# Performance work log

Measured on AMD Instinct MI355X. Metric: run time of the kernel, lower is better.

## Reference

```python
import jax, jax.numpy as jnp
import numpy as np

L_SEQ = 4096   # sequence length L
E = 1024       # embedding_size
NL = 8         # num_layers
H = 4 * E      # channel-mix hidden
V = 4          # LocalHilDim
LOGP_FACTOR = 0.5


def setup_inputs() -> dict:
    key = jax.random.key(0)
    ks = jax.random.split(key, 20)
    n = lambda k, shp, s=0.02: jax.random.normal(k, shp, jnp.float32) * s
    u = lambda k, shp: jax.random.uniform(k, shp, dtype=jnp.float32)
    return {
        "s": jax.random.randint(ks[0], (L_SEQ,), 0, V),
        "embed": n(ks[1], (V, E), 1.0),
        # TimeMixing params, stacked over layers
        "tm_first": jnp.log(jnp.float32(0.3)) + n(ks[2], (NL, E), 0.5),
        "tm_decay": -5.0 + 8.0 * u(ks[3], (NL, E)),
        "tm_mk": u(ks[4], (NL, E)),
        "tm_mv": u(ks[5], (NL, E)),
        "tm_mr": u(ks[6], (NL, E)),
        "tm_Wk": n(ks[7], (NL, E, E)),
        "tm_Wv": n(ks[8], (NL, E, E)),
        "tm_Wr": n(ks[9], (NL, E, E)),
        "tm_Wo": n(ks[10], (NL, E, E)),
        # ChannelMixing params
        "cm_mk": u(ks[11], (NL, E)),
        "cm_mr": u(ks[12], (NL, E)),
        "cm_Wk": n(ks[13], (NL, E, H)),
        "cm_Wr": n(ks[14], (NL, E, E)),
        "cm_Wv": n(ks[15], (NL, H, E)),
        # Neck / Head
        "neck_W": n(ks[16], (E, E)),
        "neck_b": jnp.zeros((E,), jnp.float32),
        "head_W": n(ks[17], (E, V)),
    }


def _wkv(k, v, time_first, time_decay):
    """Max-stabilized RWKV WKV recurrence over time. k,v: [L,E]."""
    z = jnp.zeros_like(k[0])
    init = (z, z, jnp.full_like(k[0], -jnp.inf))  # aa, bb, pp

    def step(carry, kv):
        aa, bb, pp = carry
        kk, vv = kv
        ww = time_first + kk
        p = jnp.maximum(pp, ww)
        e1 = jnp.exp(pp - p)
        e2 = jnp.exp(ww - p)
        out = (e1 * aa + e2 * vv) / (e1 * bb + e2)
        ww = pp - jnp.exp(time_decay)
        p = jnp.maximum(ww, kk)
        e1 = jnp.exp(ww - p)
        e2 = jnp.exp(kk - p)
        return (e1 * aa + e2 * vv, e1 * bb + e2, p), out

    _, out = jax.lax.scan(step, init, (k, v))
    return out


def _shift(x):
    # prepend zero-state row, drop last (token-shift with zero initial state)
    return jnp.concatenate([jnp.zeros_like(x[:1]), x[:-1]], axis=0)


def _block(x, p):
    # --- TimeMixing ---
    sx = _shift(x)
    kx = x * p["tm_mk"] + sx * (1 - p["tm_mk"])
    vx = x * p["tm_mv"] + sx * (1 - p["tm_mv"])
    rx = x * p["tm_mr"] + sx * (1 - p["tm_mr"])
    r = jax.nn.sigmoid(rx @ p["tm_Wr"])
    k = kx @ p["tm_Wk"]
    v = vx @ p["tm_Wv"]
    wkv = _wkv(k, v, p["tm_first"], p["tm_decay"])
    x = x + (r * wkv) @ p["tm_Wo"]
    # --- ChannelMixing ---
    sx = _shift(x)
    xk = x * p["cm_mk"] + sx * (1 - p["cm_mk"])
    xr = x * p["cm_mr"] + sx * (1 - p["cm_mr"])
    r = jax.nn.sigmoid(xr @ p["cm_Wr"])
    kk = jnp.square(jax.nn.relu(xk @ p["cm_Wk"]))  # [L, 4E]
    x = x + r * (kk @ p["cm_Wv"])
    return x


def reference(s, embed, tm_first, tm_decay, tm_mk, tm_mv, tm_mr,
              tm_Wk, tm_Wv, tm_Wr, tm_Wo, cm_mk, cm_mr, cm_Wk, cm_Wr, cm_Wv,
              neck_W, neck_b, head_W):
    tok = jnp.pad(s[:-1], (1, 0))
    x = embed[tok]                          # [L, E]
    layer_params = {
        "tm_first": tm_first, "tm_decay": tm_decay,
        "tm_mk": tm_mk, "tm_mv": tm_mv, "tm_mr": tm_mr,
        "tm_Wk": tm_Wk, "tm_Wv": tm_Wv, "tm_Wr": tm_Wr, "tm_Wo": tm_Wo,
        "cm_mk": cm_mk, "cm_mr": cm_mr,
        "cm_Wk": cm_Wk, "cm_Wr": cm_Wr, "cm_Wv": cm_Wv,
    }

    def body(x, p):
        return _block(x, p), None

    x, _ = jax.lax.scan(body, x, layer_params)  # scan over NL layers
    x = jax.nn.gelu(x @ neck_W + neck_b)
    logits = x @ head_W                         # [L, V]
    logp = jax.nn.log_softmax(logits) * LOGP_FACTOR
    # log-amplitude of configuration s (Q is None -> no mask, no penalty)
    return jnp.take_along_axis(logp, s[:, None], axis=-1).sum(axis=-2).squeeze(-1)
```

## Files before the change

### kernel.cpp

```cpp
#include <hip/hip_runtime.h>
#include <stdint.h>

#define L_SEQ 4096
#define EDIM  1024
#define HDIM  4096
#define NLAY  8
#define WKV_C 128
#define WKV_T 32
#define SCAN_LANES 16
#define SCAN_CPT   (WKV_C / SCAN_LANES)

typedef unsigned short u16;
typedef __attribute__((ext_vector_type(8))) short short8;
typedef __attribute__((ext_vector_type(4))) float f32x4;
typedef __attribute__((ext_vector_type(4))) unsigned short us4;
typedef __attribute__((ext_vector_type(8))) unsigned short us8;

static __device__ __forceinline__ u16 f2b(float f) {
  union { float f; uint32_t u; } a; a.f = f;
  uint32_t u = a.u;
  return (u16)((u + 0x7FFFu + ((u >> 16) & 1u)) >> 16);
}
static __device__ __forceinline__ float b2f(u16 b) {
  union { uint32_t u; float f; } a; a.u = ((uint32_t)b) << 16;
  return a.f;
}
static __device__ __forceinline__ float sigm(float v) {
  return 1.f / (1.f + __expf(-v));
}
static __device__ __forceinline__ float4 ld_bf4(const u16* __restrict__ p, size_t i) {
  us4 v = *reinterpret_cast<const us4*>(&p[i]);
  return make_float4(b2f(v.x), b2f(v.y), b2f(v.z), b2f(v.w));
}

static __device__ __forceinline__ void gld_lds16(const void* g, void* l) {
  __builtin_amdgcn_global_load_lds(
      (const __attribute__((address_space(1))) void*)g,
      (__attribute__((address_space(3))) void*)l, 16, 0, 0);
}


__global__ void k_f0(const int* __restrict__ s, const float* __restrict__ embed,
                     const float* __restrict__ mk, const float* __restrict__ mv,
                     const float* __restrict__ mr, u16* __restrict__ xA,
                     u16* __restrict__ kx, u16* __restrict__ vx, u16* __restrict__ rx) {
  int i = (blockIdx.x * blockDim.x + threadIdx.x) * 4;
  int t = i >> 10, e = i & 1023;
  int tok = (t == 0) ? 0 : s[t - 1];
  float4 xc = *reinterpret_cast<const float4*>(&embed[tok * EDIM + e]);
  float4 xs = make_float4(0.f, 0.f, 0.f, 0.f);
  if (t > 0) {
    int tokp = (t == 1) ? 0 : s[t - 2];
    xs = *reinterpret_cast<const float4*>(&embed[tokp * EDIM + e]);
  }
  us4 ox; ox.x = f2b(xc.x); ox.y = f2b(xc.y); ox.z = f2b(xc.z); ox.w = f2b(xc.w);
  *reinterpret_cast<us4*>(&xA[i]) = ox;
  float4 m; us4 o;
  m = *reinterpret_cast<const float4*>(&mk[e]);
  o.x = f2b(xc.x * m.x + xs.x * (1.f - m.x)); o.y = f2b(xc.y * m.y + xs.y * (1.f - m.y));
  o.z = f2b(xc.z * m.z + xs.z * (1.f - m.z)); o.w = f2b(xc.w * m.w + xs.w * (1.f - m.w));
  *reinterpret_cast<us4*>(&kx[i]) = o;
  m = *reinterpret_cast<const float4*>(&mv[e]);
  o.x = f2b(xc.x * m.x + xs.x * (1.f - m.x)); o.y = f2b(xc.y * m.y + xs.y * (1.f - m.y));
  o.z = f2b(xc.z * m.z + xs.z * (1.f - m.z)); o.w = f2b(xc.w * m.w + xs.w * (1.f - m.w));
  *reinterpret_cast<us4*>(&vx[i]) = o;
  m = *reinterpret_cast<const float4*>(&mr[e]);
  o.x = f2b(xc.x * m.x + xs.x * (1.f - m.x)); o.y = f2b(xc.y * m.y + xs.y * (1.f - m.y));
  o.z = f2b(xc.z * m.z + xs.z * (1.f - m.z)); o.w = f2b(xc.w * m.w + xs.w * (1.f - m.w));
  *reinterpret_cast<us4*>(&rx[i]) = o;
}

static __device__ __forceinline__ float4 cm_finish(const u16* __restrict__ xB,
                                                   const u16* __restrict__ PR,
                                                   const u16* __restrict__ PB, int i) {
  const size_t LE = (size_t)L_SEQ * EDIM;
  float4 xm = ld_bf4(xB, i);
  float4 r0 = ld_bf4(PR, i), r1 = ld_bf4(PR, i + LE);
  float4 v0 = ld_bf4(PB, i), v1 = ld_bf4(PB, i + LE);
  float4 v2 = ld_bf4(PB, i + 2 * LE), v3 = ld_bf4(PB, i + 3 * LE);
  xm.x += sigm(r0.x + r1.x) * (v0.x + v1.x + v2.x + v3.x);
  xm.y += sigm(r0.y + r1.y) * (v0.y + v1.y + v2.y + v3.y);
  xm.z += sigm(r0.z + r1.z) * (v0.z + v1.z + v2.z + v3.z);
  xm.w += sigm(r0.w + r1.w) * (v0.w + v1.w + v2.w + v3.w);
  return xm;
}

__global__ void k_f1(const u16* __restrict__ xB, const u16* __restrict__ PR,
                     const u16* __restrict__ PB,
                     const float* __restrict__ mk, const float* __restrict__ mv,
                     const float* __restrict__ mr, u16* __restrict__ xA,
                     u16* __restrict__ kx, u16* __restrict__ vx, u16* __restrict__ rx) {
  int i = (blockIdx.x * blockDim.x + threadIdx.x) * 4;
  int e = i & 1023;
  float4 xc = cm_finish(xB, PR, PB, i);
  float4 xs = make_float4(0.f, 0.f, 0.f, 0.f);
  if (i >= EDIM) xs = cm_finish(xB, PR, PB, i - EDIM);
  us4 ox; ox.x = f2b(xc.x); ox.y = f2b(xc.y); ox.z = f2b(xc.z); ox.w = f2b(xc.w);
  *reinterpret_cast<us4*>(&xA[i]) = ox;
  float4 m; us4 o;
  m = *reinterpret_cast<const float4*>(&mk[e]);
  o.x = f2b(xc.x * m.x + xs.x * (1.f - m.x)); o.y = f2b(xc.y * m.y + xs.y * (1.f - m.y));
  o.z = f2b(xc.z * m.z + xs.z * (1.f - m.z)); o.w = f2b(xc.w * m.w + xs.w * (1.f - m.w));
  *reinterpret_cast<us4*>(&kx[i]) = o;
  m = *reinterpret_cast<const float4*>(&mv[e]);
  o.x = f2b(xc.x * m.x + xs.x * (1.f - m.x)); o.y = f2b(xc.y * m.y + xs.y * (1.f - m.y));
  o.z = f2b(xc.z * m.z + xs.z * (1.f - m.z)); o.w = f2b(xc.w * m.w + xs.w * (1.f - m.w));
  *reinterpret_cast<us4*>(&vx[i]) = o;
  m = *reinterpret_cast<const float4*>(&mr[e]);
  o.x = f2b(xc.x * m.x + xs.x * (1.f - m.x)); o.y = f2b(xc.y * m.y + xs.y * (1.f - m.y));
  o.z = f2b(xc.z * m.z + xs.z * (1.f - m.z)); o.w = f2b(xc.w * m.w + xs.w * (1.f - m.w));
  *reinterpret_cast<us4*>(&rx[i]) = o;
}

static __device__ __forceinline__ float4 tm_finish(const u16* __restrict__ xA,
                                                   const u16* __restrict__ PA, int i) {
  const size_t LE = (size_t)L_SEQ * EDIM;
  float4 xm = ld_bf4(xA, i);
  float4 a = ld_bf4(PA, i), b = ld_bf4(PA, i + LE);
  xm.x += a.x + b.x; xm.y += a.y + b.y; xm.z += a.z + b.z; xm.w += a.w + b.w;
  return xm;
}

__global__ void k_f2(const u16* __restrict__ xA, const u16* __restrict__ PA,
                     const float* __restrict__ mk, const float* __restrict__ mr,
                     u16* __restrict__ xB, u16* __restrict__ kx, u16* __restrict__ rx) {
  int i = (blockIdx.x * blockDim.x + threadIdx.x) * 4;
  int e = i & 1023;
  float4 xc = tm_finish(xA, PA, i);
  float4 xs = make_float4(0.f, 0.f, 0.f, 0.f);
  if (i >= EDIM) xs = tm_finish(xA, PA, i - EDIM);
  us4 ox; ox.x = f2b(xc.x); ox.y = f2b(xc.y); ox.z = f2b(xc.z); ox.w = f2b(xc.w);
  *reinterpret_cast<us4*>(&xB[i]) = ox;
  float4 m; us4 o;
  m = *reinterpret_cast<const float4*>(&mk[e]);
  o.x = f2b(xc.x * m.x + xs.x * (1.f - m.x)); o.y = f2b(xc.y * m.y + xs.y * (1.f - m.y));
  o.z = f2b(xc.z * m.z + xs.z * (1.f - m.z)); o.w = f2b(xc.w * m.w + xs.w * (1.f - m.w));
  *reinterpret_cast<us4*>(&kx[i]) = o;
  m = *reinterpret_cast<const float4*>(&mr[e]);
  o.x = f2b(xc.x * m.x + xs.x * (1.f - m.x)); o.y = f2b(xc.y * m.y + xs.y * (1.f - m.y));
  o.z = f2b(xc.z * m.z + xs.z * (1.f - m.z)); o.w = f2b(xc.w * m.w + xs.w * (1.f - m.w));
  *reinterpret_cast<us4*>(&rx[i]) = o;
}

__global__ void k_f3(const u16* __restrict__ xB, const u16* __restrict__ PR,
                     const u16* __restrict__ PB, u16* __restrict__ hb) {
  int i = (blockIdx.x * blockDim.x + threadIdx.x) * 4;
  float4 xc = cm_finish(xB, PR, PB, i);
  us4 o;
  o.x = f2b(xc.x); o.y = f2b(xc.y); o.z = f2b(xc.z); o.w = f2b(xc.w);
  *reinterpret_cast<us4*>(&hb[i]) = o;
}

static __device__ __forceinline__ float gelu1(float v) {
  float c = 0.7978845608028654f * (v + 0.044715f * v * v * v);
  return 0.5f * v * (1.f + tanhf(c));
}

static __device__ __forceinline__
void tconv2(const float* __restrict__ s, u16* __restrict__ d, int K, int N,
            int n0, int k0) {
  __shared__ float tile[64][65];
  int tid = threadIdx.x;
  int tx = tid & 15, ty = tid >> 4;
#pragma unroll
  for (int i = 0; i < 4; ++i) {
    int kr = ty + i * 16;
    float4 v = *reinterpret_cast<const float4*>(&s[(size_t)(k0 + kr) * N + n0 + tx * 4]);
    tile[kr][tx * 4 + 0] = v.x; tile[kr][tx * 4 + 1] = v.y;
    tile[kr][tx * 4 + 2] = v.z; tile[kr][tx * 4 + 3] = v.w;
  }
  __syncthreads();
  int tx8 = tid & 7, ny = tid >> 3;
#pragma unroll
  for (int h = 0; h < 2; ++h) {
    int n = ny + h * 32;
    us8 o;
#pragma unroll
    for (int c = 0; c < 8; ++c) o[c] = f2b(tile[tx8 * 8 + c][n]);
    *reinterpret_cast<us8*>(&d[(size_t)(n0 + n) * K + k0 + tx8 * 8]) = o;
  }
}

__global__ __launch_bounds__(256)
void k_tconv(const float* __restrict__ src, u16* __restrict__ dst, int K, int N) {
  tconv2(src + (size_t)blockIdx.z * K * N, dst + (size_t)blockIdx.z * K * N,
         K, N, blockIdx.x * 64, blockIdx.y * 64);
}

#define TC_EE  (41 * 256)
#define TC_EH  8192
__global__ __launch_bounds__(256)
void k_tconv_all(const float* __restrict__ Wk, const float* __restrict__ Wv,
                 const float* __restrict__ Wr, const float* __restrict__ Wo,
                 const float* __restrict__ cWr, const float* __restrict__ nW,
                 const float* __restrict__ cWk, const float* __restrict__ cWv,
                 u16* __restrict__ oWk, u16* __restrict__ oWv, u16* __restrict__ oWr,
                 u16* __restrict__ oWo, u16* __restrict__ ocWr, u16* __restrict__ onW,
                 u16* __restrict__ ocWk, u16* __restrict__ ocWv) {
  const size_t EE = (size_t)EDIM * EDIM, EH = (size_t)EDIM * HDIM;
  int bid = blockIdx.x;
  if (bid < TC_EE) {
    int z = bid >> 8, rem = bid & 255;
    const float* src; u16* dst;
    if (z < 8)       { src = Wk  + (size_t)z * EE;        dst = oWk  + (size_t)z * EE; }
    else if (z < 16) { src = Wv  + (size_t)(z - 8) * EE;  dst = oWv  + (size_t)(z - 8) * EE; }
    else if (z < 24) { src = Wr  + (size_t)(z - 16) * EE; dst = oWr  + (size_t)(z - 16) * EE; }
    else if (z < 32) { src = Wo  + (size_t)(z - 24) * EE; dst = oWo  + (size_t)(z - 24) * EE; }
    else if (z < 40) { src = cWr + (size_t)(z - 32) * EE; dst = ocWr + (size_t)(z - 32) * EE; }
    else             { src = nW;                          dst = onW; }
    tconv2(src, dst, EDIM, EDIM, (rem & 15) * 64, (rem >> 4) * 64);
  } else if (bid < TC_EE + TC_EH) {
    int b = bid - TC_EE;
    int z = b >> 10, rem = b & 1023;
    tconv2(cWk + (size_t)z * EH, ocWk + (size_t)z * EH, EDIM, HDIM,
           (rem & 63) * 64, (rem >> 6) * 64);
  } else {
    int b = bid - TC_EE - TC_EH;
    int z = b >> 10, rem = b & 1023;
    tconv2(cWv + (size_t)z * EH, ocWv + (size_t)z * EH, HDIM, EDIM,
           (rem & 15) * 64, (rem >> 4) * 64);
  }
}

template <int EPI>
__device__ __forceinline__
void g256_body(const u16* __restrict__ A, const u16* __restrict__ Bt,
               void* __restrict__ Cv, int N, int ldk, int klen,
               int bm, int bn) {
  extern __shared__ __align__(16) u16 lds[];
  const int tid = threadIdx.x, lane = tid & 63, w = tid >> 6;
  const int wr = w >> 2, wc = w & 3;
  const int l16 = lane & 15, lhi = lane >> 4;
  const int NT = klen >> 5;

  f32x4 acc[8][4];
#pragma unroll
  for (int i = 0; i < 8; ++i)
#pragma unroll
    for (int j = 0; j < 4; ++j)
#pragma unroll
      for (int r = 0; r < 4; ++r) acc[i][j][r] = 0.f;

  const int sd = tid * 16;
  const int sr = sd >> 6;
  const int sc = ((sd >> 4) & 3) ^ ((sr >> 1) & 3);
  const int sdst = w * 512;

  const int spn = lhi ^ ((l16 >> 1) & 3);
  const int aBase = wr * 4096 + l16 * 32 + spn * 8;
  const int bBase = 8192 + (wc >> 1) * 4096 + ((wc & 1) * 64 + l16) * 32 + spn * 8;

  auto stage_ht = [&](int kt, int ht) {
    const u16* src = (ht < 2) ? A : Bt;
    int rowbase = ((ht < 2) ? bm : bn) + (ht & 1) * 128;
    gld_lds16(src + (size_t)(rowbase + sr) * ldk + kt * 32 + sc * 8,
              &lds[(kt & 3) * 16384 + ht * 4096 + sdst]);
  };

#pragma unroll
  for (int t = 0; t < 3; ++t)
#pragma unroll
    for (int h = 0; h < 4; ++h) stage_ht(t, h);
  asm volatile("s_waitcnt vmcnt(8)" ::: "memory");
  __builtin_amdgcn_s_barrier();

  short8 a[4], b[4];
  for (int kt = 0; kt < NT; ++kt) {
    const int pb = (kt & 3) * 16384;
    __builtin_amdgcn_sched_barrier(0);
#pragma unroll
    for (int mi = 0; mi < 4; ++mi)
      a[mi] = *reinterpret_cast<const short8*>(&lds[pb + aBase + mi * 512]);
#pragma unroll
    for (int ni = 0; ni < 4; ++ni)
      b[ni] = *reinterpret_cast<const short8*>(&lds[pb + bBase + ni * 512]);
    if (kt + 3 < NT) { stage_ht(kt + 3, 0); stage_ht(kt + 3, 1); }
    __builtin_amdgcn_s_barrier();
    asm volatile("s_waitcnt lgkmcnt(0)" ::: "memory");
    __builtin_amdgcn_sched_barrier(0);
    __builtin_amdgcn_s_setprio(1);
#pragma unroll
    for (int mi = 0; mi < 4; ++mi)
#pragma unroll
      for (int ni = 0; ni < 4; ++ni)
        acc[mi][ni] = __builtin_amdgcn_mfma_f32_16x16x32_bf16(a[mi], b[ni], acc[mi][ni], 0, 0, 0);
    __builtin_amdgcn_s_setprio(0);
    __builtin_amdgcn_s_barrier();
    __builtin_amdgcn_sched_barrier(0);
#pragma unroll
    for (int mi = 0; mi < 4; ++mi)
      a[mi] = *reinterpret_cast<const short8*>(&lds[pb + aBase + 2048 + mi * 512]);
    if (kt + 3 < NT) { stage_ht(kt + 3, 2); stage_ht(kt + 3, 3); }
    __builtin_amdgcn_s_barrier();
    asm volatile("s_waitcnt lgkmcnt(0)" ::: "memory");
    __builtin_amdgcn_sched_barrier(0);
    __builtin_amdgcn_s_setprio(1);
#pragma unroll
    for (int mi = 0; mi < 4; ++mi)
#pragma unroll
      for (int ni = 0; ni < 4; ++ni)
        acc[4 + mi][ni] = __builtin_amdgcn_mfma_f32_16x16x32_bf16(a[mi], b[ni], acc[4 + mi][ni], 0, 0, 0);
    __builtin_amdgcn_s_setprio(0);
    if (kt + 4 <= NT)      asm volatile("s_waitcnt vmcnt(8)" ::: "memory");
    else if (kt + 3 == NT) asm volatile("s_waitcnt vmcnt(4)" ::: "memory");
    else if (kt + 2 == NT) asm volatile("s_waitcnt vmcnt(0)" ::: "memory");
    __builtin_amdgcn_s_barrier();
  }

#pragma unroll
  for (int q = 0; q < 8; ++q)
#pragma unroll
    for (int ni = 0; ni < 4; ++ni)
#pragma unroll
      for (int r = 0; r < 4; ++r) {
        int row = bm + wr * 128 + (q >> 2) * 64 + (q & 3) * 16 + lhi * 4 + r;
        int col = bn + wc * 64 + ni * 16 + l16;
        size_t o = (size_t)row * N + col;
        float v = acc[q][ni][r];
        if constexpr (EPI == 0) ((float*)Cv)[o] = v;
        else if constexpr (EPI == 1) ((u16*)Cv)[o] = f2b(v);
        else { v = fmaxf(v, 0.f); ((u16*)Cv)[o] = f2b(v * v); }
      }
}

__global__ __launch_bounds__(512)
void k_g256_cmk(const u16* __restrict__ A, const u16* __restrict__ Bt,
                u16* __restrict__ C) {
  int bid = blockIdx.x;
  int wg = (bid & 7) * 32 + (bid >> 3);
  int lb = wg & 3, sv = wg >> 2;
  int by = (sv >> 3) * 2 + (lb & 1);
  int bx = (sv & 7) * 2 + (lb >> 1);
  g256_body<2>(A, Bt, C, HDIM, EDIM, EDIM, by * 256, bx * 256);
}

__global__ __launch_bounds__(512)
void k_g256_wv(const u16* __restrict__ A, const u16* __restrict__ Bt,
               u16* __restrict__ P) {
  int bid = blockIdx.x;
  int wg = (bid & 7) * 32 + (bid >> 3);
  int z = wg >> 6, rem = wg & 63;
  int lb = rem & 3, sv = rem >> 2;
  int by = (sv >> 1) * 2 + (lb & 1);
  int bx = (sv & 1) * 2 + (lb >> 1);
  g256_body<1>(A + z * 1024, Bt + z * 1024, P + (size_t)z * L_SEQ * EDIM,
               EDIM, HDIM, 1024, by * 256, bx * 256);
}

__global__ __launch_bounds__(512)
void k_g256_3(const u16* __restrict__ A0, const u16* __restrict__ A1, const u16* __restrict__ A2,
              const u16* __restrict__ B0, const u16* __restrict__ B1, const u16* __restrict__ B2,
              u16* __restrict__ C0, u16* __restrict__ C1, u16* __restrict__ C2) {
  int bid = blockIdx.x;
  int wg = (bid & 7) * 24 + (bid >> 3);
  int z = wg >> 6, rem = wg & 63;
  int lb = rem & 3, sv = rem >> 2;
  int by = (sv >> 1) * 2 + (lb & 1);
  int bx = (sv & 1) * 2 + (lb >> 1);
  const u16* A = (z == 0) ? A0 : (z == 1) ? A1 : A2;
  const u16* B = (z == 0) ? B0 : (z == 1) ? B1 : B2;
  u16*       C = (z == 0) ? C0 : (z == 1) ? C1 : C2;
  g256_body<1>(A, B, C, EDIM, EDIM, EDIM, by * 256, bx * 256);
}

__device__ __forceinline__
void gemm_body(const u16* __restrict__ A, const u16* __restrict__ Bt,
               u16* __restrict__ Cv, int N, int ldk, int klen, int bm, int bn) {
  __shared__ __align__(16) u16 As[4][128 * 32];
  __shared__ __align__(16) u16 Bs[4][128 * 32];
  const int tid = threadIdx.x, lane = tid & 63, w = tid >> 6;
  const int wr = w >> 1, wc = w & 1;
  const int l16 = lane & 15, lhi = lane >> 4;

  f32x4 acc[4][4];
#pragma unroll
  for (int a = 0; a < 4; ++a)
#pragma unroll
    for (int b = 0; b < 4; ++b)
#pragma unroll
      for (int r = 0; r < 4; ++r) acc[a][b][r] = 0.f;

  const size_t rowBytes = (size_t)ldk * 2;
  const int NT = klen >> 5;

  int srow[2], scb[2], ldso[2];
#pragma unroll
  for (int i = 0; i < 2; ++i) {
    int off = w * 2048 + i * 1024 + lane * 16;
    int r = off >> 6, sl = (off >> 4) & 3;
    srow[i] = r;
    scb[i] = ((sl - (r >> 1)) & 3) << 4;
    ldso[i] = (w * 2048 + i * 1024) >> 1;
  }

  auto stage = [&](int t, int buf) {
    int kb = t * 64;
#pragma unroll
    for (int i = 0; i < 2; ++i) {
      gld_lds16((const char*)A + (size_t)(bm + srow[i]) * rowBytes + kb + scb[i],
                &As[buf][ldso[i]]);
      gld_lds16((const char*)Bt + (size_t)(bn + srow[i]) * rowBytes + kb + scb[i],
                &Bs[buf][ldso[i]]);
    }
  };

  int aoff[4], boff[4];
#pragma unroll
  for (int mi = 0; mi < 4; ++mi) {
    int r = wr * 64 + mi * 16 + l16;
    aoff[mi] = r * 32 + (((lhi + (r >> 1)) & 3) << 3);
    r = wc * 64 + mi * 16 + l16;
    boff[mi] = r * 32 + (((lhi + (r >> 1)) & 3) << 3);
  }

  stage(0, 0); stage(1, 1); stage(2, 2);
  for (int t = 0; t < NT; ++t) {
    const int cur = t & 3;
    if (t + 2 < NT)      asm volatile("s_waitcnt vmcnt(8)" ::: "memory");
    else if (t + 1 < NT) asm volatile("s_waitcnt vmcnt(4)" ::: "memory");
    else                 asm volatile("s_waitcnt vmcnt(0)" ::: "memory");
    __builtin_amdgcn_s_barrier();
    __builtin_amdgcn_sched_barrier(0);
    short8 af[4], bfr[4];
#pragma unroll
    for (int mi = 0; mi < 4; ++mi)
      af[mi] = *reinterpret_cast<const short8*>(&As[cur][aoff[mi]]);
#pragma unroll
    for (int ni = 0; ni < 4; ++ni)
      bfr[ni] = *reinterpret_cast<const short8*>(&Bs[cur][boff[ni]]);
    if (t + 3 < NT) stage(t + 3, (t + 3) & 3);
    asm volatile("s_waitcnt lgkmcnt(0)" ::: "memory");
    __builtin_amdgcn_sched_barrier(0);
#pragma unroll
    for (int mi = 0; mi < 4; ++mi)
#pragma unroll
      for (int ni = 0; ni < 4; ++ni)
        acc[mi][ni] = __builtin_amdgcn_mfma_f32_16x16x32_bf16(af[mi], bfr[ni], acc[mi][ni], 0, 0, 0);
  }
#pragma unroll
  for (int mi = 0; mi < 4; ++mi)
#pragma unroll
    for (int ni = 0; ni < 4; ++ni)
#pragma unroll
      for (int r = 0; r < 4; ++r) {
        int row = bm + wr * 64 + mi * 16 + lhi * 4 + r;
        int col = bn + wc * 64 + ni * 16 + l16;
        Cv[(size_t)row * N + col] = f2b(acc[mi][ni][r]);
      }
}

__global__ __launch_bounds__(256)
void k_gemm_sk2(const u16* __restrict__ A, const u16* __restrict__ Bt,
                u16* __restrict__ P, int K) {
  const int z = blockIdx.z, klen = K >> 1;
  gemm_body(A + z * klen, Bt + z * klen, P + (size_t)z * L_SEQ * EDIM,
            EDIM, K, klen, blockIdx.y * 128, blockIdx.x * 128);
}


__global__ void k_wkv_pass1(const u16* __restrict__ k, const u16* __restrict__ v,
                            const float* __restrict__ w_,
                            float* __restrict__ sa, float* __restrict__ sb,
                            float* __restrict__ sp) {
  int id = blockIdx.x * blockDim.x + threadIdx.x;
  int e = id & 1023, c = id >> 10;
  float D = __expf(w_[e]);
  float aa = 0.f, bb = 0.f, pp = -__builtin_inff();
  const u16* kp = k + (size_t)c * WKV_T * EDIM + e;
  const u16* vp = v + (size_t)c * WKV_T * EDIM + e;
#pragma unroll 4
  for (int i = 0; i < WKV_T; ++i) {
    float kk = b2f(kp[i * EDIM]), vv = b2f(vp[i * EDIM]);
    float ww = pp - D;
    float p2 = fmaxf(ww, kk);
    float e1 = __expf(ww - p2), e2 = __expf(kk - p2);
    aa = e1 * aa + e2 * vv;
    bb = e1 * bb + e2;
    pp = p2;
  }
  sa[id] = aa; sb[id] = bb; sp[id] = pp;
}

__global__ __launch_bounds__(256)
void k_wkv_scan16(const float* __restrict__ w_,
                  const float* __restrict__ sa, const float* __restrict__ sb,
                  const float* __restrict__ sp,
                  float* __restrict__ oa, float* __restrict__ ob,
                  float* __restrict__ op) {
  int t = blockIdx.x * blockDim.x + threadIdx.x;
  int e = t >> 4, j = t & (SCAN_LANES - 1);
  const float NEG = -1e30f;
  float DT = __expf(w_[e]) * (float)WKV_T;
  float Ea[SCAN_CPT], Eb[SCAN_CPT], Ep[SCAN_CPT];
  float A = 0.f, B = 0.f, P = NEG;
  int base = j * SCAN_CPT;
#pragma unroll
  for (int i = 0; i < SCAN_CPT; ++i) {
    int idx = (base + i) * EDIM + e;
    Ea[i] = A; Eb[i] = B; Ep[i] = P;
    float a = sa[idx], b = sb[idx], q = sp[idx];
    float shift = P - DT;
    float pn = fmaxf(shift, q);
    float w1 = __expf(shift - pn), w2 = __expf(q - pn);
    A = w1 * A + w2 * a; B = w1 * B + w2 * b; P = pn;
  }
  float tA = A, tB = B, tP = P; int tn = SCAN_CPT;
#pragma unroll
  for (int d = 1; d < SCAN_LANES; d <<= 1) {
    float fA = __shfl_up(tA, d, SCAN_LANES);
    float fB = __shfl_up(tB, d, SCAN_LANES);
    float fP = __shfl_up(tP, d, SCAN_LANES);
    int   fn = __shfl_up(tn, d, SCAN_LANES);
    if (j >= d) {
      float shift = fP - DT * (float)tn;
      float pn = fmaxf(shift, tP);
      float w1 = __expf(shift - pn), w2 = __expf(tP - pn);
      tA = w1 * fA + w2 * tA; tB = w1 * fB + w2 * tB; tP = pn; tn += fn;
    }
  }
  float pA = __shfl_up(tA, 1, SCAN_LANES);
  float pB = __shfl_up(tB, 1, SCAN_LANES);
  float pP = __shfl_up(tP, 1, SCAN_LANES);
  if (j == 0) { pA = 0.f; pB = 0.f; pP = NEG; }
#pragma unroll
  for (int i = 0; i < SCAN_CPT; ++i) {
    float shift = pP - DT * (float)i;
    float pn = fmaxf(shift, Ep[i]);
    float w1 = __expf(shift - pn), w2 = __expf(Ep[i] - pn);
    int idx = (base + i) * EDIM + e;
    oa[idx] = w1 * pA + w2 * Ea[i];
    ob[idx] = w1 * pB + w2 * Eb[i];
    op[idx] = pn;
  }
}

__global__ void k_wkv_pass2(const u16* __restrict__ k, const u16* __restrict__ v,
                            const float* __restrict__ u_, const float* __restrict__ w_,
                            const float* __restrict__ sa, const float* __restrict__ sb,
                            const float* __restrict__ sp,
                            const u16* __restrict__ rpre, u16* __restrict__ rwb) {
  int id = blockIdx.x * blockDim.x + threadIdx.x;
  int e = id & 1023, c = id >> 10;
  float u = u_[e];
  float D = __expf(w_[e]);
  float aa = sa[id], bb = sb[id], pp = sp[id];
  const size_t base = (size_t)c * WKV_T * EDIM + e;
  const u16* kp = k + base;
  const u16* vp = v + base;
  const u16* rp = rpre + base;
  u16* op = rwb + base;
#pragma unroll 4
  for (int i = 0; i < WKV_T; ++i) {
    float kk = b2f(kp[i * EDIM]), vv = b2f(vp[i * EDIM]);
    float ww = u + kk;
    float p = fmaxf(pp, ww);
    float e1 = __expf(pp - p), e2 = __expf(ww - p);
    float out = (e1 * aa + e2 * vv) / (e1 * bb + e2);
    op[i * EDIM] = f2b(out * sigm(b2f(rp[i * EDIM])));
    float w2s = pp - D;
    float p2 = fmaxf(w2s, kk);
    float e1b = __expf(w2s - p2), e2b = __expf(kk - p2);
    aa = e1b * aa + e2b * vv;
    bb = e1b * bb + e2b;
    pp = p2;
  }
}

__global__ __launch_bounds__(256)
void k_head(const u16* __restrict__ P, const float* __restrict__ nb,
            const float* __restrict__ W,
            const int* __restrict__ s, float* __restrict__ partial) {
  const size_t LE = (size_t)L_SEQ * EDIM;
  int t = blockIdx.x, tid = threadIdx.x;
  float a0 = 0.f, a1 = 0.f, a2 = 0.f, a3 = 0.f;
  for (int e = tid; e < EDIM; e += 256) {
    size_t i = (size_t)t * EDIM + e;
    float hv = gelu1(b2f(P[i]) + b2f(P[i + LE]) + nb[e]);
    const float4 wv = *reinterpret_cast<const float4*>(W + e * 4);
    a0 += hv * wv.x; a1 += hv * wv.y; a2 += hv * wv.z; a3 += hv * wv.w;
  }
#pragma unroll
  for (int off = 32; off > 0; off >>= 1) {
    a0 += __shfl_down(a0, off, 64);
    a1 += __shfl_down(a1, off, 64);
    a2 += __shfl_down(a2, off, 64);
    a3 += __shfl_down(a3, off, 64);
  }
  __shared__ float sm[4][4];
  int w = tid >> 6, lane = tid & 63;
  if (lane == 0) { sm[w][0] = a0; sm[w][1] = a1; sm[w][2] = a2; sm[w][3] = a3; }
  __syncthreads();
  if (tid == 0) {
    float lg[4];
#pragma unroll
    for (int j = 0; j < 4; ++j) lg[j] = sm[0][j] + sm[1][j] + sm[2][j] + sm[3][j];
    float m = fmaxf(fmaxf(lg[0], lg[1]), fmaxf(lg[2], lg[3]));
    float sum = expf(lg[0] - m) + expf(lg[1] - m) + expf(lg[2] - m) + expf(lg[3] - m);
    partial[t] = 0.5f * (lg[s[t]] - m - logf(sum));
  }
}

__global__ __launch_bounds__(256)
void k_reduce(const float* __restrict__ partial, float* __restrict__ out) {
  int tid = threadIdx.x;
  float a = 0.f;
  for (int j = tid; j < L_SEQ; j += 256) a += partial[j];
#pragma unroll
  for (int off = 32; off > 0; off >>= 1) a += __shfl_down(a, off, 64);
  __shared__ float sm[4];
  if ((tid & 63) == 0) sm[tid >> 6] = a;
  __syncthreads();
  if (tid == 0) out[0] = sm[0] + sm[1] + sm[2] + sm[3];
}


extern "C" void kernel_launch(void* const* d_in, const int* in_sizes, int n_in,
                              void* d_out, int out_size, void* d_ws, size_t ws_size,
                              hipStream_t stream) {
  const int*   s        = (const int*)d_in[0];
  const float* embed    = (const float*)d_in[1];
  const float* tm_first = (const float*)d_in[2];
  const float* tm_decay = (const float*)d_in[3];
  const float* tm_mk    = (const float*)d_in[4];
  const float* tm_mv    = (const float*)d_in[5];
  const float* tm_mr    = (const float*)d_in[6];
  const float* tm_Wk    = (const float*)d_in[7];
  const float* tm_Wv    = (const float*)d_in[8];
  const float* tm_Wr    = (const float*)d_in[9];
  const float* tm_Wo    = (const float*)d_in[10];
  const float* cm_mk    = (const float*)d_in[11];
  const float* cm_mr    = (const float*)d_in[12];
  const float* cm_Wk    = (const float*)d_in[13];
  const float* cm_Wr    = (const float*)d_in[14];
  const float* cm_Wv    = (const float*)d_in[15];
  const float* neck_W   = (const float*)d_in[16];
  const float* neck_b   = (const float*)d_in[17];
  const float* head_W   = (const float*)d_in[18];

  char* ws = (char*)d_ws;
  size_t off = 0;
  auto alloc = [&](size_t bytes) { char* p = ws + off; off += (bytes + 255) & ~(size_t)255; return p; };
  const size_t LE2 = (size_t)L_SEQ * EDIM * 2;
  const size_t EE  = (size_t)EDIM * EDIM, EH = (size_t)EDIM * HDIM;

  u16*   xA    = (u16*)alloc(LE2);
  u16*   xB    = (u16*)alloc(LE2);
  u16*   kxb   = (u16*)alloc(LE2);
  u16*   vxb   = (u16*)alloc(LE2);
  u16*   rxb   = (u16*)alloc(LE2);
  u16*   kf    = (u16*)alloc(LE2);
  u16*   vf    = (u16*)alloc(LE2);
  u16*   rpre  = (u16*)alloc(LE2);
  u16*   kkb   = (u16*)alloc((size_t)L_SEQ * HDIM * 2);
  u16*   PA    = (u16*)alloc(2 * LE2);
  u16*   PR    = (u16*)alloc(2 * LE2);
  u16*   PB    = (u16*)alloc(4 * LE2);
  float* partial = (float*)alloc((size_t)L_SEQ * 4);
  float* sa  = (float*)alloc((size_t)WKV_C * EDIM * 4);
  float* sb  = (float*)alloc((size_t)WKV_C * EDIM * 4);
  float* sp  = (float*)alloc((size_t)WKV_C * EDIM * 4);
  float* sa2 = (float*)alloc((size_t)WKV_C * EDIM * 4);
  float* sb2 = (float*)alloc((size_t)WKV_C * EDIM * 4);
  float* sp2 = (float*)alloc((size_t)WKV_C * EDIM * 4);

  size_t remain = (ws_size > off) ? ws_size - off : 0;
  const size_t bigNeed = (5 * EE * NLAY + 2 * EH * NLAY + EE) * 2 + 16 * 256;
  const bool big = remain >= bigNeed;
  const int NB = big ? NLAY : 1;
  u16* wWk   = (u16*)alloc(EE * NB * 2);
  u16* wWv   = (u16*)alloc(EE * NB * 2);
  u16* wWr   = (u16*)alloc(EE * NB * 2);
  u16* wWo   = (u16*)alloc(EE * NB * 2);
  u16* wcmWr = (u16*)alloc(EE * NB * 2);
  u16* wcmWk = (u16*)alloc(EH * NB * 2);
  u16* wcmWv = (u16*)alloc(EH * NB * 2);
  u16* wneck = big ? (u16*)alloc(EE * 2) : wWk;

  const dim3 blk(256);
  const dim3 blk512(512);
  const dim3 gE4((L_SEQ * EDIM) / 1024);
  const dim3 gemmSK(EDIM / 128, L_SEQ / 128, 2);
  const dim3 gWkv((WKV_C * EDIM) / 256);
  const dim3 gScan((EDIM * SCAN_LANES) / 256);
  const size_t DLDS = 131072;

  if (big) {
    k_tconv_all<<<dim3(TC_EE + 2 * TC_EH), blk, 0, stream>>>(
        tm_Wk, tm_Wv, tm_Wr, tm_Wo, cm_Wr, neck_W, cm_Wk, cm_Wv,
        wWk, wWv, wWr, wWo, wcmWr, wneck, wcmWk, wcmWv);
  }

  for (int l = 0; l < NLAY; ++l) {
    size_t oE  = (size_t)l * EDIM;
    size_t oEE = (size_t)l * EE;
    size_t oEH = (size_t)l * EH;
    size_t wE  = big ? oEE : 0;
    size_t wH  = big ? oEH : 0;
    if (!big) {
      k_tconv<<<dim3(EDIM / 64, EDIM / 64, 1), blk, 0, stream>>>(tm_Wk + oEE, wWk, EDIM, EDIM);
      k_tconv<<<dim3(EDIM / 64, EDIM / 64, 1), blk, 0, stream>>>(tm_Wv + oEE, wWv, EDIM, EDIM);
      k_tconv<<<dim3(EDIM / 64, EDIM / 64, 1), blk, 0, stream>>>(tm_Wr + oEE, wWr, EDIM, EDIM);
      k_tconv<<<dim3(EDIM / 64, EDIM / 64, 1), blk, 0, stream>>>(tm_Wo + oEE, wWo, EDIM, EDIM);
      k_tconv<<<dim3(EDIM / 64, EDIM / 64, 1), blk, 0, stream>>>(cm_Wr + oEE, wcmWr, EDIM, EDIM);
      k_tconv<<<dim3(HDIM / 64, EDIM / 64, 1), blk, 0, stream>>>(cm_Wk + oEH, wcmWk, EDIM, HDIM);
      k_tconv<<<dim3(EDIM / 64, HDIM / 64, 1), blk, 0, stream>>>(cm_Wv + oEH, wcmWv, HDIM, EDIM);
    }
    if (l == 0)
      k_f0<<<gE4, blk, 0, stream>>>(s, embed, tm_mk + oE, tm_mv + oE, tm_mr + oE,
                                    xA, kxb, vxb, rxb);
    else
      k_f1<<<gE4, blk, 0, stream>>>(xB, PR, PB, tm_mk + oE, tm_mv + oE, tm_mr + oE,
                                    xA, kxb, vxb, rxb);
    k_g256_3<<<dim3(192), blk512, DLDS, stream>>>(kxb, vxb, rxb,
                                                  wWk + wE, wWv + wE, wWr + wE,
                                                  kf, vf, rpre);
    k_wkv_pass1<<<gWkv, blk, 0, stream>>>(kf, vf, tm_decay + oE, sa, sb, sp);
    k_wkv_scan16<<<gScan, blk, 0, stream>>>(tm_decay + oE, sa, sb, sp, sa2, sb2, sp2);
    k_wkv_pass2<<<gWkv, blk, 0, stream>>>(kf, vf, tm_first + oE, tm_decay + oE,
                                          sa2, sb2, sp2, rpre, vxb);
    k_gemm_sk2<<<gemmSK, blk, 0, stream>>>(vxb, wWo + wE, PA, EDIM);
    k_f2<<<gE4, blk, 0, stream>>>(xA, PA, cm_mk + oE, cm_mr + oE, xB, kxb, rxb);
    k_gemm_sk2<<<gemmSK, blk, 0, stream>>>(rxb, wcmWr + wE, PR, EDIM);
    k_g256_cmk<<<dim3(256), blk512, DLDS, stream>>>(kxb, wcmWk + wH, kkb);
    k_g256_wv<<<dim3(256), blk512, DLDS, stream>>>(kkb, wcmWv + wH, PB);
  }
  if (!big) k_tconv<<<dim3(EDIM / 64, EDIM / 64, 1), blk, 0, stream>>>(neck_W, wneck, EDIM, EDIM);
  k_f3<<<gE4, blk, 0, stream>>>(xB, PR, PB, kxb);
  k_gemm_sk2<<<gemmSK, blk, 0, stream>>>(kxb, wneck, PA, EDIM);
  k_head<<<dim3(L_SEQ), blk, 0, stream>>>(PA, neck_b, head_W, s, partial);
  k_reduce<<<dim3(1), blk, 0, stream>>>(partial, (float*)d_out);

  (void)in_sizes; (void)n_in; (void)out_size;
}
```

Measured before the change: 1.849 ms.

## Replace split-K 128x128 GEMM with 256x128 tile, 512-thread pipelined kernel

Replaces the E x E split-K GEMM, which used 128x128 tiles and 256 threads, with a 256x128 tile kernel on 512 threads (8 waves in a 2x4 layout). It uses dynamic LDS with a 4-stage ring, XOR-swizzled layout, split half-tile loads interleaved with MFMA, s_setprio around the MFMA blocks, and an XCD-aware block remap over 256 blocks. The goal is more reuse per tile and better overlap of global loads with compute for the Wo, cm_Wr and neck projections. The cost is more barriers per K step and 96KB of LDS per block, which may limit occupancy.

```diff
diff --git a/kernel.cpp b/kernel.cpp
--- a/kernel.cpp
+++ b/kernel.cpp
@@ -364,97 +364,111 @@
 }
 
 __device__ __forceinline__
-void gemm_body(const u16* __restrict__ A, const u16* __restrict__ Bt,
-               u16* __restrict__ Cv, int N, int ldk, int klen, int bm, int bn) {
-  __shared__ __align__(16) u16 As[4][128 * 32];
-  __shared__ __align__(16) u16 Bs[4][128 * 32];
+void g128_body(const u16* __restrict__ A, const u16* __restrict__ Bt,
+               u16* __restrict__ Cv, int N, int ldk, int klen,
+               int bm, int bn) {
+  extern __shared__ __align__(16) u16 lds[];
   const int tid = threadIdx.x, lane = tid & 63, w = tid >> 6;
-  const int wr = w >> 1, wc = w & 1;
+  const int wr = w >> 2, wc = w & 3;
   const int l16 = lane & 15, lhi = lane >> 4;
-
-  f32x4 acc[4][4];
-#pragma unroll
-  for (int a = 0; a < 4; ++a)
-#pragma unroll
-    for (int b = 0; b < 4; ++b)
-#pragma unroll
-      for (int r = 0; r < 4; ++r) acc[a][b][r] = 0.f;
-
-  const size_t rowBytes = (size_t)ldk * 2;
   const int NT = klen >> 5;
 
-  int srow[2], scb[2], ldso[2];
-#pragma unroll
-  for (int i = 0; i < 2; ++i) {
-    int off = w * 2048 + i * 1024 + lane * 16;
-    int r = off >> 6, sl = (off >> 4) & 3;
-    srow[i] = r;
-    scb[i] = ((sl - (r >> 1)) & 3) << 4;
-    ldso[i] = (w * 2048 + i * 1024) >> 1;
-  }
-
-  auto stage = [&](int t, int buf) {
-    int kb = t * 64;
-#pragma unroll
-    for (int i = 0; i < 2; ++i) {
-      gld_lds16((const char*)A + (size_t)(bm + srow[i]) * rowBytes + kb + scb[i],
-                &As[buf][ldso[i]]);
-      gld_lds16((const char*)Bt + (size_t)(bn + srow[i]) * rowBytes + kb + scb[i],
-                &Bs[buf][ldso[i]]);
-    }
+  f32x4 acc[8][2];
+#pragma unroll
+  for (int i = 0; i < 8; ++i)
+#pragma unroll
+    for (int j = 0; j < 2; ++j)
+#pragma unroll
+      for (int r = 0; r < 4; ++r) acc[i][j][r] = 0.f;
+
+  const int sd = tid * 16;
+  const int sr = sd >> 6;
+  const int sc = ((sd >> 4) & 3) ^ ((sr >> 1) & 3);
+  const int sdst = w * 512;
+
+  const int spn = lhi ^ ((l16 >> 1) & 3);
+  const int aBase = wr * 4096 + l16 * 32 + spn * 8;
+  const int bBase = 8192 + (wc * 32 + l16) * 32 + spn * 8;
+
+  auto stage_ht = [&](int kt, int ht) {
+    const u16* src = (ht < 2) ? A : Bt;
+    int rowbase = (ht < 2) ? (bm + ht * 128) : bn;
+    int dsto = (ht < 2) ? ht * 4096 : 8192;
+    gld_lds16(src + (size_t)(rowbase + sr) * ldk + kt * 32 + sc * 8,
+              &lds[(kt & 3) * 12288 + dsto + sdst]);
   };
 
-  int aoff[4], boff[4];
-#pragma unroll
-  for (int mi = 0; mi < 4; ++mi) {
-    int r = wr * 64 + mi * 16 + l16;
-    aoff[mi] = r * 32 + (((lhi + (r >> 1)) & 3) << 3);
-    r = wc * 64 + mi * 16 + l16;
-    boff[mi] = r * 32 + (((lhi + (r >> 1)) & 3) << 3);
-  }
-
-  stage(0, 0); stage(1, 1); stage(2, 2);
-  for (int t = 0; t < NT; ++t) {
-    const int cur = t & 3;
-    if (t + 2 < NT)      asm volatile("s_waitcnt vmcnt(8)" ::: "memory");
-    else if (t + 1 < NT) asm volatile("s_waitcnt vmcnt(4)" ::: "memory");
-    else                 asm volatile("s_waitcnt vmcnt(0)" ::: "memory");
+#pragma unroll
+  for (int t = 0; t < 3; ++t) {
+    stage_ht(t, 0); stage_ht(t, 1); stage_ht(t, 2);
+  }
+  asm volatile("s_waitcnt vmcnt(6)" ::: "memory");
+  __builtin_amdgcn_s_barrier();
+
+  short8 a[4], b[2];
+  for (int kt = 0; kt < NT; ++kt) {
+    const int pb = (kt & 3) * 12288;
+    __builtin_amdgcn_sched_barrier(0);
+#pragma unroll
+    for (int mi = 0; mi < 4; ++mi)
+      a[mi] = *reinterpret_cast<const short8*>(&lds[pb + aBase + mi * 512]);
+#pragma unroll
+    for (int ni = 0; ni < 2; ++ni)
+      b[ni] = *reinterpret_cast<const short8*>(&lds[pb + bBase + ni * 512]);
+    if (kt + 3 < NT) { stage_ht(kt + 3, 0); stage_ht(kt + 3, 1); }
+    __builtin_amdgcn_s_barrier();
+    asm volatile("s_waitcnt lgkmcnt(0)" ::: "memory");
+    __builtin_amdgcn_sched_barrier(0);
+    __builtin_amdgcn_s_setprio(1);
+#pragma unroll
+    for (int mi = 0; mi < 4; ++mi)
+#pragma unroll
+      for (int ni = 0; ni < 2; ++ni)
+        acc[mi][ni] = __builtin_amdgcn_mfma_f32_16x16x32_bf16(a[mi], b[ni], acc[mi][ni], 0, 0, 0);
+    __builtin_amdgcn_s_setprio(0);
     __builtin_amdgcn_s_barrier();
     __builtin_amdgcn_sched_barrier(0);
-    short8 af[4], bfr[4];
 #pragma unroll
     for (int mi = 0; mi < 4; ++mi)
-      af[mi] = *reinterpret_cast<const short8*>(&As[cur][aoff[mi]]);
-#pragma unroll
-    for (int ni = 0; ni < 4; ++ni)
-      bfr[ni] = *reinterpret_cast<const short8*>(&Bs[cur][boff[ni]]);
-    if (t + 3 < NT) stage(t + 3, (t + 3) & 3);
+      a[mi] = *reinterpret_cast<const short8*>(&lds[pb + aBase + 2048 + mi * 512]);
+    if (kt + 3 < NT) stage_ht(kt + 3, 2);
+    __builtin_amdgcn_s_barrier();
     asm volatile("s_waitcnt lgkmcnt(0)" ::: "memory");
     __builtin_amdgcn_sched_barrier(0);
+    __builtin_amdgcn_s_setprio(1);
 #pragma unroll
     for (int mi = 0; mi < 4; ++mi)
 #pragma unroll
-      for (int ni = 0; ni < 4; ++ni)
-        acc[mi][ni] = __builtin_amdgcn_mfma_f32_16x16x32_bf16(af[mi], bfr[ni], acc[mi][ni], 0, 0, 0);
-  }
-#pragma unroll
-  for (int mi = 0; mi < 4; ++mi)
-#pragma unroll
-    for (int ni = 0; ni < 4; ++ni)
+      for (int ni = 0; ni < 2; ++ni)
+        acc[4 + mi][ni] = __builtin_amdgcn_mfma_f32_16x16x32_bf16(a[mi], b[ni], acc[4 + mi][ni], 0, 0, 0);
+    __builtin_amdgcn_s_setprio(0);
+    if (kt + 4 <= NT)      asm volatile("s_waitcnt vmcnt(6)" ::: "memory");
+    else if (kt + 3 == NT) asm volatile("s_waitcnt vmcnt(3)" ::: "memory");
+    else if (kt + 2 == NT) asm volatile("s_waitcnt vmcnt(0)" ::: "memory");
+    __builtin_amdgcn_s_barrier();
+  }
+
+#pragma unroll
+  for (int q = 0; q < 8; ++q)
+#pragma unroll
+    for (int ni = 0; ni < 2; ++ni)
 #pragma unroll
       for (int r = 0; r < 4; ++r) {
-        int row = bm + wr * 64 + mi * 16 + lhi * 4 + r;
-        int col = bn + wc * 64 + ni * 16 + l16;
-        Cv[(size_t)row * N + col] = f2b(acc[mi][ni][r]);
+        int row = bm + wr * 128 + (q >> 2) * 64 + (q & 3) * 16 + lhi * 4 + r;
+        int col = bn + wc * 32 + ni * 16 + l16;
+        Cv[(size_t)row * N + col] = f2b(acc[q][ni][r]);
       }
 }
 
-__global__ __launch_bounds__(256)
-void k_gemm_sk2(const u16* __restrict__ A, const u16* __restrict__ Bt,
-                u16* __restrict__ P, int K) {
-  const int z = blockIdx.z, klen = K >> 1;
-  gemm_body(A + z * klen, Bt + z * klen, P + (size_t)z * L_SEQ * EDIM,
-            EDIM, K, klen, blockIdx.y * 128, blockIdx.x * 128);
+__global__ __launch_bounds__(512)
+void k_gx128_sk2(const u16* __restrict__ A, const u16* __restrict__ Bt,
+                 u16* __restrict__ P) {
+  int bid = blockIdx.x;
+  int wg = (bid & 7) * 32 + (bid >> 3);
+  int z = wg >> 7, rem = wg & 127;
+  int by = rem >> 3, bx = rem & 7;
+  g128_body(A + z * 512, Bt + z * 512, P + (size_t)z * L_SEQ * EDIM,
+            EDIM, EDIM, 512, by * 256, bx * 128);
 }
 
 
@@ -679,10 +693,10 @@
   const dim3 blk(256);
   const dim3 blk512(512);
   const dim3 gE4((L_SEQ * EDIM) / 1024);
-  const dim3 gemmSK(EDIM / 128, L_SEQ / 128, 2);
   const dim3 gWkv((WKV_C * EDIM) / 256);
   const dim3 gScan((EDIM * SCAN_LANES) / 256);
-  const size_t DLDS = 131072;
+  const size_t DLDS  = 131072;
+  const size_t DLDS2 = 98304;
 
   if (big) {
     k_tconv_all<<<dim3(TC_EE + 2 * TC_EH), blk, 0, stream>>>(
@@ -718,15 +732,15 @@
     k_wkv_scan16<<<gScan, blk, 0, stream>>>(tm_decay + oE, sa, sb, sp, sa2, sb2, sp2);
     k_wkv_pass2<<<gWkv, blk, 0, stream>>>(kf, vf, tm_first + oE, tm_decay + oE,
                                           sa2, sb2, sp2, rpre, vxb);
-    k_gemm_sk2<<<gemmSK, blk, 0, stream>>>(vxb, wWo + wE, PA, EDIM);
+    k_gx128_sk2<<<dim3(256), blk512, DLDS2, stream>>>(vxb, wWo + wE, PA);
     k_f2<<<gE4, blk, 0, stream>>>(xA, PA, cm_mk + oE, cm_mr + oE, xB, kxb, rxb);
-    k_gemm_sk2<<<gemmSK, blk, 0, stream>>>(rxb, wcmWr + wE, PR, EDIM);
+    k_gx128_sk2<<<dim3(256), blk512, DLDS2, stream>>>(rxb, wcmWr + wE, PR);
     k_g256_cmk<<<dim3(256), blk512, DLDS, stream>>>(kxb, wcmWk + wH, kkb);
     k_g256_wv<<<dim3(256), blk512, DLDS, stream>>>(kkb, wcmWv + wH, PB);
   }
   if (!big) k_tconv<<<dim3(EDIM / 64, EDIM / 64, 1), blk, 0, stream>>>(neck_W, wneck, EDIM, EDIM);
   k_f3<<<gE4, blk, 0, stream>>>(xB, PR, PB, kxb);
-  k_gemm_sk2<<<gemmSK, blk, 0, stream>>>(kxb, wneck, PA, EDIM);
+  k_gx128_sk2<<<dim3(256), blk512, DLDS2, stream>>>(kxb, wneck, PA);
   k_head<<<dim3(L_SEQ), blk, 0, stream>>>(PA, neck_b, head_W, s, partial);
   k_reduce<<<dim3(1), blk, 0, stream>>>(partial, (float*)d_out);
 
```

After: 1.778 ms. 3.8% less time.
